# Kernel tuning notes

Measured on AMD Instinct MI355X. Metric: run time of the kernel, lower is better.

Reference implementation:

```python
import jax, jax.numpy as jnp
import numpy as np

N = 20000          # nodes
E = 320000         # edges
IN_C = 512         # input features
HID = 512          # 2*out_channels (first GCN layer width)
OUT = 256          # out_channels == num_hidden
PROJ = 256         # num_proj_hidden


def _gcn_conv(x, W, b, src, dst):
    """PyG GCNConv: x' = D^{-1/2}(A+I)D^{-1/2} X W + b (self-loops added)."""
    n = x.shape[0]
    x = x @ W  # [N, F_out]
    ones = jnp.ones((src.shape[0],), x.dtype)
    deg = jax.ops.segment_sum(ones, dst, num_segments=n) + 1.0  # +1 self-loop
    dis = jax.lax.rsqrt(deg)
    coef = dis[src] * dis[dst]                      # [E]
    agg = jax.ops.segment_sum(x[src] * coef[:, None], dst, num_segments=n)
    agg = agg + x * (dis * dis)[:, None]            # self-loop messages
    return agg + b


def setup_inputs() -> dict:
    key = jax.random.key(0)
    ks = jax.random.split(key, 12)
    s = 0.02
    return {
        "node_features": jax.random.normal(ks[0], (N, IN_C), jnp.float32),
        "edge_index": jax.random.randint(ks[1], (2, E), 0, N, jnp.int64),
        "W1": jax.random.normal(ks[2], (IN_C, HID), jnp.float32) * s,
        "b1": jnp.zeros((HID,), jnp.float32),
        "W2": jax.random.normal(ks[3], (HID, OUT), jnp.float32) * s,
        "b2": jnp.zeros((OUT,), jnp.float32),
        "a": jnp.asarray(0.25, jnp.float32),  # shared PReLU weight
        "W3": jax.random.normal(ks[4], (OUT, PROJ), jnp.float32) * s,
        "b3": jnp.zeros((PROJ,), jnp.float32),
        "W4": jax.random.normal(ks[5], (PROJ, OUT), jnp.float32) * s,
        "b4": jnp.zeros((OUT,), jnp.float32),
    }


def reference(node_features, edge_index, W1, b1, W2, b2, a, W3, b3, W4, b4):
    src, dst = edge_index[0], edge_index[1]
    prelu = lambda x: jnp.where(x > 0, x, a * x)
    h = prelu(_gcn_conv(node_features, W1, b1, src, dst))
    h = prelu(_gcn_conv(h, W2, b2, src, dst))
    # projection MLP: Linear -> ELU -> Linear
    h2 = jax.nn.elu(h @ W3 + b3)
    return h2 @ W4 + b4
```

## Files before the change

### kernel.cpp

```cpp
#include <hip/hip_runtime.h>
#include <stdint.h>

typedef unsigned short u16;
typedef unsigned int   u32;
typedef __attribute__((ext_vector_type(8))) short short8;
typedef __attribute__((ext_vector_type(4))) float f32x4;

__device__ __forceinline__ float bf2f(u16 h){
    return __uint_as_float(((u32)h) << 16);
}
__device__ __forceinline__ u16 f2bf(float f){
    u32 u = __float_as_uint(f);
    u += 0x7fffu + ((u >> 16) & 1u);
    return (u16)(u >> 16);
}

__device__ __forceinline__ void gl_lds16(const void* g, void* l){
    __builtin_amdgcn_global_load_lds(
        (__attribute__((address_space(1))) void*)(uintptr_t)g,
        (__attribute__((address_space(3))) void*)(uintptr_t)l,
        16, 0, 0);
}

#define CAP 96

__global__ void prep_all(const void* w1, const void* w2, const void* w3,
                         const void* w4, const void* X,
                         const void* b1, const void* b2, const void* b3,
                         const void* b4, const void* av,
                         const int* __restrict__ EI, int* __restrict__ cnt,
                         int* __restrict__ buck, int E,
                         u16* o1, u16* o2, u16* o3, u16* o4,
                         u16* xbf, u16* d1, u16* d2, u16* d3, u16* d4,
                         u16* da, int NN){
    __shared__ int sf;
    __shared__ u16 tb[32][33];
    int lt = threadIdx.y * 32 + threadIdx.x;

    if (blockIdx.z == 5){
        if (lt == 0) sf = 0;
        __syncthreads();
        if (EI[2*lt + 1] != 0) atomicOr(&sf, 1);
        __syncthreads();
        int fmt = sf;
        for (int e = (blockIdx.y * 16 + blockIdx.x) * 256 + lt; e < E; e += 65536){
            int d = fmt ? EI[E + e] : EI[2*(E + e)];
            if ((unsigned)d < (unsigned)NN){
                int slot = atomicAdd(&cnt[d], 1);
                if (slot < CAP) buck[(size_t)d * CAP + slot] = fmt ? EI[e] : EI[2*e];
            }
        }
        return;
    }

    if (lt == 0) sf = 0;
    __syncthreads();
    {
        int huge = 0;
        const u16* w = (const u16*)w1;
        #pragma unroll
        for (int k = 0; k < 8; k++){
            u16 h = w[lt * 8 + k];
            if (((h >> 7) & 0xFF) >= 0x7F) huge = 1;
        }
        if (huge) atomicOr(&sf, 1);
    }
    __syncthreads();
    int f32 = sf;

    if (blockIdx.z == 4){
        #define CV(s,i) (f32 ? f2bf(((const float*)(s))[i]) : ((const u16*)(s))[i])
        if (blockIdx.x == 0 && blockIdx.y == 0){
            d1[lt]       = CV(b1, lt);
            d1[lt + 256] = CV(b1, lt + 256);
            d2[lt] = CV(b2, lt);
            d3[lt] = CV(b3, lt);
            d4[lt] = CV(b4, lt);
            if (lt == 0) da[0] = CV(av, 0);
        }
        #undef CV
        size_t nb8 = (size_t)NN * 64;
        size_t step = 256u * 256u;
        for (size_t i = (size_t)(blockIdx.y * 16 + blockIdx.x) * 256 + lt; i < nb8; i += step){
            short8 o;
            if (f32){
                const float* p = (const float*)X + i * 8;
                f32x4 a0 = *(const f32x4*)p;
                f32x4 a1 = *(const f32x4*)(p + 4);
                #pragma unroll
                for (int j = 0; j < 4; j++){
                    o[j]     = (short)f2bf(a0[j]);
                    o[4 + j] = (short)f2bf(a1[j]);
                }
            } else {
                o = *(const short8*)((const u16*)X + i * 8);
            }
            *(short8*)(xbf + i * 8) = o;
        }
        return;
    }

    const void* in; u16* out; int K, N;
    switch (blockIdx.z){
        case 0:  in = w1; out = o1; K = 512; N = 512; break;
        case 1:  in = w2; out = o2; K = 512; N = 256; break;
        case 2:  in = w3; out = o3; K = 256; N = 256; break;
        default: in = w4; out = o4; K = 256; N = 256; break;
    }
    int bx = blockIdx.x * 32;
    int by = blockIdx.y * 32;
    if (bx >= N || by >= K) return;
    int x = threadIdx.x, y = threadIdx.y;
    #pragma unroll
    for (int i = 0; i < 32; i += 8){
        size_t idx = (size_t)(by + y + i) * N + bx + x;
        tb[y + i][x] = f32 ? f2bf(((const float*)in)[idx]) : ((const u16*)in)[idx];
    }
    __syncthreads();
    #pragma unroll
    for (int i = 0; i < 32; i += 8)
        out[(size_t)(bx + y + i) * K + by + x] = tb[x][y + i];
}

#define GTN 128
#define GBK 64

template<int MODE, int OUTF>
__global__ __launch_bounds__(256) void gemm128(
    const u16* __restrict__ A, const u16* __restrict__ BT,
    const u16* __restrict__ bias, void* __restrict__ Cv,
    int M, int K, int N, int nN,
    const int* __restrict__ cntp, float* __restrict__ disp,
    int* __restrict__ buckp, float* __restrict__ cdisp)
{
    __shared__ __align__(16) u16 As[128 * GBK];
    __shared__ __align__(16) u16 Bs[GTN * GBK];
    if (cntp){
        int stride = gridDim.x * 256;
        int gid = blockIdx.x * 256 + (int)threadIdx.x;
        for (int i = gid; i < M; i += stride)
            disp[i] = rsqrtf((float)cntp[i] + 1.0f);
        int tot = M * CAP;
        for (int i = gid; i < tot; i += stride){
            int n = i / CAP;
            int s = i - n * CAP;
            int deg = cntp[n]; if (deg > CAP) deg = CAP;
            int ng8 = (deg + 7) & ~7;
            if (s < deg){
                cdisp[i] = rsqrtf((float)cntp[buckp[i]] + 1.0f);
            } else if (s < ng8){
                cdisp[i] = 0.f;
                buckp[i] = buckp[(size_t)n * CAP + deg - 1];
            }
        }
    }
    int nwg = gridDim.x;
    int flat = blockIdx.x;
    int q8 = nwg >> 3, r8 = nwg & 7;
    int xcd = flat & 7, idx8 = flat >> 3;
    int wg = (xcd < r8 ? xcd * (q8 + 1) : r8 * (q8 + 1) + (xcd - r8) * q8) + idx8;
    int bm = (wg / nN) * 128;
    int bn = (wg % nN) * GTN;

    int tid  = threadIdx.x;
    int lane = tid & 63;
    int wm   = (tid >> 7) & 1;
    int wn   = (tid >> 6) & 1;

    f32x4 acc[4][4] = {};

    int srow = tid >> 3;
    int scol = (tid & 7) * 8;
    const u16* aP = A  + (size_t)(bm + srow) * K + scol;
    const u16* bP = BT + (size_t)(bn + srow) * K + scol;
    u16* lA = &As[tid * 8];
    u16* lB = &Bs[tid * 8];

    int q   = lane >> 4;
    int r16 = lane & 15;
    const u16* ra = &As[(wm*64 + r16) * GBK + q*8];
    const u16* rb = &Bs[(wn*64 + r16) * GBK + q*8];

    for (int k0 = 0; k0 < K; k0 += GBK){
        #pragma unroll
        for (int r = 0; r < 4; r++){
            gl_lds16(aP + (size_t)r*32*K + k0, lA + r*32*GBK);
            gl_lds16(bP + (size_t)r*32*K + k0, lB + r*32*GBK);
        }
        __syncthreads();
        #pragma unroll
        for (int kk = 0; kk < 2; kk++){
            short8 af[4], bf[4];
            #pragma unroll
            for (int i = 0; i < 4; i++) af[i] = *(const short8*)(ra + i*16*GBK + kk*32);
            #pragma unroll
            for (int j = 0; j < 4; j++) bf[j] = *(const short8*)(rb + j*16*GBK + kk*32);
            #pragma unroll
            for (int i = 0; i < 4; i++)
                #pragma unroll
                for (int j = 0; j < 4; j++)
                    acc[i][j] = __builtin_amdgcn_mfma_f32_16x16x32_bf16(af[i], bf[j], acc[i][j], 0, 0, 0);
        }
        __syncthreads();
    }

    int q4 = q * 4;
    #pragma unroll
    for (int i = 0; i < 4; i++){
        #pragma unroll
        for (int j = 0; j < 4; j++){
            int gcol = bn + wn*64 + j*16 + r16;
            float bvv = (MODE >= 1) ? bf2f(bias[gcol]) : 0.f;
            #pragma unroll
            for (int r = 0; r < 4; r++){
                int grow = bm + wm*64 + i*16 + q4 + r;
                if (grow < M){
                    float v = acc[i][j][r] + bvv;
                    if (MODE == 2) v = (v > 0.f) ? v : expm1f(v);
                    if (OUTF) ((float*)Cv)[(size_t)grow * N + gcol] = v;
                    else      ((u16*)Cv)[(size_t)grow * N + gcol] = f2bf(v);
                }
            }
        }
    }
}

__global__ __launch_bounds__(256) void gemm34(
    const u16* __restrict__ Q, const u16* __restrict__ W3T,
    const u16* __restrict__ W4T, const u16* __restrict__ b3,
    const u16* __restrict__ b4, float* __restrict__ OUT, int M)
{
    __shared__ __align__(16) u16 As[64 * 64];
    __shared__ __align__(16) u16 Bs[256 * 64];
    __shared__ __align__(16) u16 T[64 * 256];
    int nwg = gridDim.x;
    int flat = blockIdx.x;
    int q8 = nwg >> 3, r8 = nwg & 7;
    int xcd = flat & 7, idx8 = flat >> 3;
    int wg = (xcd < r8 ? xcd * (q8 + 1) : r8 * (q8 + 1) + (xcd - r8) * q8) + idx8;
    int bm = wg * 64;

    int tid  = threadIdx.x;
    int lane = tid & 63;
    int wm   = (tid >> 7) & 1;
    int wn   = (tid >> 6) & 1;
    int q    = lane >> 4;
    int r16  = lane & 15;
    int q4   = q * 4;
    int srow = tid >> 3;
    int scol = (tid & 7) * 8;

    u16* lA = &As[tid * 8];
    u16* lB = &Bs[tid * 8];
    const u16* ra = &As[(wm*32 + r16) * 64 + q*8];
    const u16* rb = &Bs[(wn*128 + r16) * 64 + q*8];

    f32x4 acc[2][8];

    #pragma unroll
    for (int i = 0; i < 2; i++)
        #pragma unroll
        for (int j = 0; j < 8; j++) acc[i][j] = (f32x4){0,0,0,0};
    {
        const u16* aP = Q   + (size_t)(bm + srow) * 256 + scol;
        const u16* bP = W3T + (size_t)srow * 256 + scol;
        for (int ks = 0; ks < 4; ks++){
            int k0 = ks * 64;
            #pragma unroll
            for (int r = 0; r < 2; r++)
                gl_lds16(aP + (size_t)r*32*256 + k0, lA + r*32*64);
            #pragma unroll
            for (int r = 0; r < 8; r++)
                gl_lds16(bP + (size_t)r*32*256 + k0, lB + r*32*64);
            __syncthreads();
            #pragma unroll
            for (int kk = 0; kk < 2; kk++){
                short8 af[2], bf[8];
                #pragma unroll
                for (int i = 0; i < 2; i++) af[i] = *(const short8*)(ra + i*16*64 + kk*32);
                #pragma unroll
                for (int j = 0; j < 8; j++) bf[j] = *(const short8*)(rb + j*16*64 + kk*32);
                #pragma unroll
                for (int i = 0; i < 2; i++)
                    #pragma unroll
                    for (int j = 0; j < 8; j++)
                        acc[i][j] = __builtin_amdgcn_mfma_f32_16x16x32_bf16(af[i], bf[j], acc[i][j], 0, 0, 0);
            }
            __syncthreads();
        }
    }
    #pragma unroll
    for (int i = 0; i < 2; i++){
        #pragma unroll
        for (int j = 0; j < 8; j++){
            int lc = wn*128 + j*16 + r16;
            float bvv = bf2f(b3[lc]);
            #pragma unroll
            for (int r = 0; r < 4; r++){
                int lr = wm*32 + i*16 + q4 + r;
                float v = acc[i][j][r] + bvv;
                v = (v > 0.f) ? v : expm1f(v);
                T[lr * 256 + lc] = f2bf(v);
            }
        }
    }
    __syncthreads();

    #pragma unroll
    for (int i = 0; i < 2; i++)
        #pragma unroll
        for (int j = 0; j < 8; j++) acc[i][j] = (f32x4){0,0,0,0};
    {
        const u16* bP = W4T + (size_t)srow * 256 + scol;
        for (int ks = 0; ks < 4; ks++){
            int k0 = ks * 64;
            #pragma unroll
            for (int r = 0; r < 8; r++)
                gl_lds16(bP + (size_t)r*32*256 + k0, lB + r*32*64);
            __syncthreads();
            #pragma unroll
            for (int kk = 0; kk < 2; kk++){
                short8 af[2], bf[8];
                #pragma unroll
                for (int i = 0; i < 2; i++)
                    af[i] = *(const short8*)&T[(wm*32 + i*16 + r16) * 256 + k0 + kk*32 + q*8];
                #pragma unroll
                for (int j = 0; j < 8; j++) bf[j] = *(const short8*)(rb + j*16*64 + kk*32);
                #pragma unroll
                for (int i = 0; i < 2; i++)
                    #pragma unroll
                    for (int j = 0; j < 8; j++)
                        acc[i][j] = __builtin_amdgcn_mfma_f32_16x16x32_bf16(af[i], bf[j], acc[i][j], 0, 0, 0);
            }
            __syncthreads();
        }
    }
    #pragma unroll
    for (int i = 0; i < 2; i++){
        #pragma unroll
        for (int j = 0; j < 8; j++){
            int lc = wn*128 + j*16 + r16;
            float bvv = bf2f(b4[lc]);
            #pragma unroll
            for (int r = 0; r < 4; r++){
                int grow = bm + wm*32 + i*16 + q4 + r;
                if (grow < M)
                    OUT[(size_t)grow * 256 + lc] = acc[i][j][r] + bvv;
            }
        }
    }
}

template<int F, int CH>
__global__ __launch_bounds__(256) void agg_b(
    const u16* __restrict__ XW, const float* __restrict__ dis,
    const int* __restrict__ cnt, const int* __restrict__ buck,
    const float* __restrict__ cdis, const u16* __restrict__ bias,
    const u16* __restrict__ aptr, u16* __restrict__ out, int N)
{
    constexpr int NCH = F / CH;
    constexpr int LPN = CH / 8;
    constexpr int NPB = 256 / LPN;
    int bid = blockIdx.x;
    int chunk = bid % NCH;
    int node = (bid / NCH) * NPB + ((int)threadIdx.x / LPN);
    if (node >= N) return;
    int tf = chunk * CH + ((int)threadIdx.x % LPN) * 8;
    float a  = bf2f(aptr[0]);
    float di = dis[node];
    int dgc = cnt[node];
    int deg = dgc < CAP ? dgc : CAP;
    const int*   bk = buck + (size_t)node * CAP;
    const float* cd = cdis + (size_t)node * CAP;
    float acc[8] = {0,0,0,0,0,0,0,0};
    int ng = (deg + 7) >> 3;
    int si[8]; float ci[8];
    if (ng > 0){
        #pragma unroll
        for (int u = 0; u < 8; u++) si[u] = bk[u];
        #pragma unroll
        for (int u = 0; u < 8; u++) ci[u] = cd[u];
    }
    for (int g = 0; g < ng; g++){
        short8 vi[8];
        #pragma unroll
        for (int u = 0; u < 8; u++)
            vi[u] = *(const short8*)(XW + (size_t)si[u] * F + tf);
        int sn[8]; float cn[8];
        bool more = (g + 1) < ng;
        if (more){
            int base = (g + 1) * 8;
            #pragma unroll
            for (int u = 0; u < 8; u++) sn[u] = bk[base + u];
            #pragma unroll
            for (int u = 0; u < 8; u++) cn[u] = cd[base + u];
        }
        #pragma unroll
        for (int u = 0; u < 8; u++)
            #pragma unroll
            for (int j = 0; j < 8; j++)
                acc[j] += ci[u] * bf2f((u16)vi[u][j]);
        if (more){
            #pragma unroll
            for (int u = 0; u < 8; u++){ si[u] = sn[u]; ci[u] = cn[u]; }
        }
    }
    {
        short8 v = *(const short8*)(XW + (size_t)node * F + tf);
        #pragma unroll
        for (int j = 0; j < 8; j++) acc[j] += di * bf2f((u16)v[j]);
    }
    short8 bv = *(const short8*)(bias + tf);
    short8 o;
    #pragma unroll
    for (int j = 0; j < 8; j++){
        float x = di * acc[j] + bf2f((u16)bv[j]);
        x = (x > 0.f) ? x : a * x;
        o[j] = (short)f2bf(x);
    }
    *(short8*)(out + (size_t)node * F + tf) = o;
}

extern "C" void kernel_launch(void* const* d_in, const int* in_sizes, int n_in,
                              void* d_out, int out_size, void* d_ws, size_t ws_size,
                              hipStream_t stream)
{
    int iX=0, iEI=1, iW1=2, ib1=3, iW2=4, ib2=5, ia=6, iW3=7, ib3=8, iW4=9, ib4=10;
    {
        int jX=-1,jEI=-1,jW1=-1,jb1=-1,jW2=-1,ja=-1,jW3=-1,jW4=-1,jb2=-1,jb3=-1,jb4=-1;
        int n64k=0, n256=0;
        for (int i = 0; i < n_in; i++){
            switch (in_sizes[i]){
                case 10240000: jX = i; break;
                case 640000:   jEI = i; break;
                case 262144:   jW1 = i; break;
                case 131072:   jW2 = i; break;
                case 512:      jb1 = i; break;
                case 1:        ja = i; break;
                case 65536:    if (n64k++ == 0) jW3 = i; else jW4 = i; break;
                case 256: {
                    int k = n256++;
                    if (k == 0) jb2 = i; else if (k == 1) jb3 = i; else jb4 = i;
                } break;
                default: break;
            }
        }
        if (jX>=0&&jEI>=0&&jW1>=0&&jb1>=0&&jW2>=0&&ja>=0&&jW3>=0&&jW4>=0&&jb2>=0&&jb3>=0&&jb4>=0){
            iX=jX; iEI=jEI; iW1=jW1; ib1=jb1; iW2=jW2; ib2=jb2; ia=ja; iW3=jW3; ib3=jb3; iW4=jW4; ib4=jb4;
        }
    }
    int N = in_sizes[iX] / 512;
    int E = in_sizes[iEI] / 2;
    const int* EI = (const int*)d_in[iEI];
    float* OUT = (float*)d_out;
    u16*   S   = (u16*)d_out;

    char* ws = (char*)d_ws;
    size_t off = 0;
    auto alloc = [&](size_t bytes)->char*{
        char* p = ws + off;
        off = (off + bytes + 255) & ~(size_t)255;
        return p;
    };
    int MP = N + 128;
    int*   cnt  = (int*)  alloc((size_t)N*4);
    float* dis  = (float*)alloc((size_t)N*4);
    int*   buck = (int*)  alloc((size_t)N*CAP*4);
    float* cdis = (float*)alloc((size_t)N*CAP*4);
    u16*   WT1  = (u16*)  alloc((size_t)512*512*2);
    u16*   WT2  = (u16*)  alloc((size_t)256*512*2);
    u16*   WT3  = (u16*)  alloc((size_t)256*256*2);
    u16*   WT4  = (u16*)  alloc((size_t)256*256*2);
    u16*   b1c  = (u16*)  alloc((size_t)512*2);
    u16*   b2c  = (u16*)  alloc((size_t)256*2);
    u16*   b3c  = (u16*)  alloc((size_t)256*2);
    u16*   b4c  = (u16*)  alloc((size_t)256*2);
    u16*   ac   = (u16*)  alloc((size_t)8*2);
    u16*   Xbf  = (u16*)  alloc((size_t)MP*512*2);
    u16*   h1   = (u16*)  alloc((size_t)MP*512*2);
    u16*   P    = (u16*)  alloc((size_t)MP*256*2);
    u16*   Q    = (u16*)  alloc((size_t)MP*256*2);
    if (ws_size < off) return;

    hipMemsetAsync(cnt, 0, (size_t)N*4, stream);

    prep_all<<<dim3(16, 16, 6), dim3(32, 8), 0, stream>>>(
        d_in[iW1], d_in[iW2], d_in[iW3], d_in[iW4], d_in[iX],
        d_in[ib1], d_in[ib2], d_in[ib3], d_in[ib4], d_in[ia],
        EI, cnt, buck, E,
        WT1, WT2, WT3, WT4, Xbf, b1c, b2c, b3c, b4c, ac, N);

    int gm128 = (N + 127) / 128;
    int gm64  = (N + 63) / 64;
    int nodeb = (N + 31) / 32;

    gemm128<0,0><<<gm128*4, 256, 0, stream>>>(Xbf, WT1, nullptr, S, N, 512, 512, 4,
                                              cnt, dis, buck, cdis);
    agg_b<512,64><<<nodeb*8, 256, 0, stream>>>(S, dis, cnt, buck, cdis, b1c, ac, h1, N);

    gemm128<0,0><<<gm128*2, 256, 0, stream>>>(h1, WT2, nullptr, P, N, 512, 256, 2,
                                              nullptr, nullptr, nullptr, nullptr);
    agg_b<256,64><<<nodeb*4, 256, 0, stream>>>(P, dis, cnt, buck, cdis, b2c, ac, Q, N);

    gemm34<<<gm64, 256, 0, stream>>>(Q, WT3, WT4, b3c, b4c, OUT, N);
}
```

Measured before the change: 262.7 us.

## Swizzle GEMM LDS tile layout and split coefficient prep into its own kernel

The GEMM's global-to-LDS loads now apply an XOR swizzle on the 16-byte column chunk keyed by row, and the MFMA fragment reads apply the matching XOR. This is meant to remove LDS bank conflicts in the fragment reads. The degree-normalisation and bucket-padding prep, previously fused into the first GEMM's prologue, moves to a separate fully parallel kernel. That adds one launch but removes the serial prologue work from the GEMM.

```diff
diff --git a/kernel.cpp b/kernel.cpp
--- a/kernel.cpp
+++ b/kernel.cpp
@@ -122,6 +122,25 @@
         out[(size_t)(bx + y + i) * K + by + x] = tb[x][y + i];
 }
 
+__global__ void coef(const int* __restrict__ cnt, int* __restrict__ buck,
+                     float* __restrict__ dis, float* __restrict__ cdis, int N){
+    int i = blockIdx.x * 256 + threadIdx.x;
+    if (i < N) dis[i] = rsqrtf((float)cnt[i] + 1.0f);
+    int tot = N * CAP;
+    if (i < tot){
+        int n = i / CAP;
+        int s = i - n * CAP;
+        int deg = cnt[n]; if (deg > CAP) deg = CAP;
+        int ng8 = (deg + 7) & ~7;
+        if (s < deg){
+            cdis[i] = rsqrtf((float)cnt[buck[i]] + 1.0f);
+        } else if (s < ng8){
+            cdis[i] = 0.f;
+            buck[i] = buck[(size_t)n * CAP + deg - 1];
+        }
+    }
+}
+
 #define GTN 128
 #define GBK 64
 
@@ -129,31 +148,10 @@
 __global__ __launch_bounds__(256) void gemm128(
     const u16* __restrict__ A, const u16* __restrict__ BT,
     const u16* __restrict__ bias, void* __restrict__ Cv,
-    int M, int K, int N, int nN,
-    const int* __restrict__ cntp, float* __restrict__ disp,
-    int* __restrict__ buckp, float* __restrict__ cdisp)
+    int M, int K, int N, int nN)
 {
     __shared__ __align__(16) u16 As[128 * GBK];
     __shared__ __align__(16) u16 Bs[GTN * GBK];
-    if (cntp){
-        int stride = gridDim.x * 256;
-        int gid = blockIdx.x * 256 + (int)threadIdx.x;
-        for (int i = gid; i < M; i += stride)
-            disp[i] = rsqrtf((float)cntp[i] + 1.0f);
-        int tot = M * CAP;
-        for (int i = gid; i < tot; i += stride){
-            int n = i / CAP;
-            int s = i - n * CAP;
-            int deg = cntp[n]; if (deg > CAP) deg = CAP;
-            int ng8 = (deg + 7) & ~7;
-            if (s < deg){
-                cdisp[i] = rsqrtf((float)cntp[buckp[i]] + 1.0f);
-            } else if (s < ng8){
-                cdisp[i] = 0.f;
-                buckp[i] = buckp[(size_t)n * CAP + deg - 1];
-            }
-        }
-    }
     int nwg = gridDim.x;
     int flat = blockIdx.x;
     int q8 = nwg >> 3, r8 = nwg & 7;
@@ -170,16 +168,17 @@
     f32x4 acc[4][4] = {};
 
     int srow = tid >> 3;
-    int scol = (tid & 7) * 8;
-    const u16* aP = A  + (size_t)(bm + srow) * K + scol;
-    const u16* bP = BT + (size_t)(bn + srow) * K + scol;
+    int scS  = (((tid & 7) ^ (srow & 7)) * 8);
+    const u16* aP = A  + (size_t)(bm + srow) * K + scS;
+    const u16* bP = BT + (size_t)(bn + srow) * K + scS;
     u16* lA = &As[tid * 8];
     u16* lB = &Bs[tid * 8];
 
     int q   = lane >> 4;
     int r16 = lane & 15;
-    const u16* ra = &As[(wm*64 + r16) * GBK + q*8];
-    const u16* rb = &Bs[(wn*64 + r16) * GBK + q*8];
+    int swz = (r16 & 7) << 4;
+    const char* raB = (const char*)&As[(wm*64 + r16) * GBK];
+    const char* rbB = (const char*)&Bs[(wn*64 + r16) * GBK];
 
     for (int k0 = 0; k0 < K; k0 += GBK){
         #pragma unroll
@@ -190,11 +189,12 @@
         __syncthreads();
         #pragma unroll
         for (int kk = 0; kk < 2; kk++){
+            int co0 = (q*16 + kk*64) ^ swz;
             short8 af[4], bf[4];
             #pragma unroll
-            for (int i = 0; i < 4; i++) af[i] = *(const short8*)(ra + i*16*GBK + kk*32);
-            #pragma unroll
-            for (int j = 0; j < 4; j++) bf[j] = *(const short8*)(rb + j*16*GBK + kk*32);
+            for (int i = 0; i < 4; i++) af[i] = *(const short8*)(raB + i*2048 + co0);
+            #pragma unroll
+            for (int j = 0; j < 4; j++) bf[j] = *(const short8*)(rbB + j*2048 + co0);
             #pragma unroll
             for (int i = 0; i < 4; i++)
                 #pragma unroll
@@ -490,16 +490,16 @@
         EI, cnt, buck, E,
         WT1, WT2, WT3, WT4, Xbf, b1c, b2c, b3c, b4c, ac, N);
 
+    coef<<<(N*CAP + 255)/256, 256, 0, stream>>>(cnt, buck, dis, cdis, N);
+
     int gm128 = (N + 127) / 128;
     int gm64  = (N + 63) / 64;
     int nodeb = (N + 31) / 32;
 
-    gemm128<0,0><<<gm128*4, 256, 0, stream>>>(Xbf, WT1, nullptr, S, N, 512, 512, 4,
-                                              cnt, dis, buck, cdis);
+    gemm128<0,0><<<gm128*4, 256, 0, stream>>>(Xbf, WT1, nullptr, S, N, 512, 512, 4);
     agg_b<512,64><<<nodeb*8, 256, 0, stream>>>(S, dis, cnt, buck, cdis, b1c, ac, h1, N);
 
-    gemm128<0,0><<<gm128*2, 256, 0, stream>>>(h1, WT2, nullptr, P, N, 512, 256, 2,
-                                              nullptr, nullptr, nullptr, nullptr);
+    gemm128<0,0><<<gm128*2, 256, 0, stream>>>(h1, WT2, nullptr, P, N, 512, 256, 2);
     agg_b<256,64><<<nodeb*4, 256, 0, stream>>>(P, dis, cnt, buck, cdis, b2c, ac, Q, N);
 
     gemm34<<<gm64, 256, 0, stream>>>(Q, WT3, WT4, b3c, b4c, OUT, N);
```

New measurement: 240.9 us. -8.3%, faster.
